# Performance work log

Measured on AMD Instinct MI355X. Metric: run time of the kernel, lower is better.

## Reference

```python
import jax, jax.numpy as jnp
import numpy as np

H = 128

def _lstm_dir(x, w_ih, w_hh, b_ih, b_hh, reverse):
    # x: [B,T,D]; w_ih: [4H,D]; w_hh: [4H,H]; gate order i,f,g,o (PyTorch)
    B = x.shape[0]
    pre = jnp.einsum('btd,gd->btg', x, w_ih) + b_ih + b_hh  # [B,T,4H]
    if reverse:
        pre = pre[:, ::-1]
    pre = jnp.swapaxes(pre, 0, 1)  # [T,B,4H]
    h0 = jnp.zeros((B, H), dtype=x.dtype)
    c0 = jnp.zeros((B, H), dtype=x.dtype)

    def step(carry, xt):
        h, c = carry
        gates = xt + h @ w_hh.T
        i, f, g, o = jnp.split(gates, 4, axis=-1)
        c = jax.nn.sigmoid(f) * c + jax.nn.sigmoid(i) * jnp.tanh(g)
        h = jax.nn.sigmoid(o) * jnp.tanh(c)
        return (h, c), h

    _, hs = jax.lax.scan(step, (h0, c0), pre)  # hs: [T,B,H]
    hs = jnp.swapaxes(hs, 0, 1)  # [B,T,H]
    if reverse:
        hs = hs[:, ::-1]
    return hs

def _bilstm_layer(x, wf, rf):
    fwd = _lstm_dir(x, *wf, reverse=False)
    bwd = _lstm_dir(x, *rf, reverse=True)
    return jnp.concatenate([fwd, bwd], axis=-1)

def setup_inputs() -> dict:
    key = jax.random.key(0)
    ks = jax.random.split(key, 32)
    s = 0.05
    d = {'x': jax.random.normal(ks[0], (64, 512, 64), dtype=jnp.float32)}
    i = 1
    for l, din in [(0, 64), (1, 2 * H)]:
        for suf in ['', 'r']:
            d[f'w_ih_l{l}{suf}'] = s * jax.random.normal(ks[i], (4 * H, din)); i += 1
            d[f'w_hh_l{l}{suf}'] = s * jax.random.normal(ks[i], (4 * H, H)); i += 1
            d[f'b_ih_l{l}{suf}'] = s * jax.random.normal(ks[i], (4 * H,)); i += 1
            d[f'b_hh_l{l}{suf}'] = s * jax.random.normal(ks[i], (4 * H,)); i += 1
    d['w_fc'] = s * jax.random.normal(ks[i], (64, 2 * H)); i += 1
    d['b_fc'] = s * jax.random.normal(ks[i], (64,))
    return d

def reference(x, w_ih_l0, w_hh_l0, b_ih_l0, b_hh_l0, w_ih_l0r, w_hh_l0r, b_ih_l0r, b_hh_l0r, w_ih_l1, w_hh_l1, b_ih_l1, b_hh_l1, w_ih_l1r, w_hh_l1r, b_ih_l1r, b_hh_l1r, w_fc, b_fc):
    h = _bilstm_layer(x, (w_ih_l0, w_hh_l0, b_ih_l0, b_hh_l0), (w_ih_l0r, w_hh_l0r, b_ih_l0r, b_hh_l0r))
    h = _bilstm_layer(h, (w_ih_l1, w_hh_l1, b_ih_l1, b_hh_l1), (w_ih_l1r, w_hh_l1r, b_ih_l1r, b_hh_l1r))
    return h @ w_fc.T + b_fc
```

## Files before the change

### kernel.cpp

```cpp
#include <hip/hip_runtime.h>

#define TT 512
#define BB 64
#define HH 128
#define G4 512
#define PF 4

typedef short bf16x8 __attribute__((ext_vector_type(8)));
typedef short s16x4  __attribute__((ext_vector_type(4)));
typedef float f32x4  __attribute__((ext_vector_type(4)));
typedef _Float16 f16x8v __attribute__((ext_vector_type(8)));

__device__ __forceinline__ unsigned short f2bf(float x) {
    unsigned u = __float_as_uint(x);
    u += 0x7fff + ((u >> 16) & 1);
    return (unsigned short)(u >> 16);
}
__device__ __forceinline__ float bf2f(unsigned short h) {
    return __uint_as_float(((unsigned)h) << 16);
}

__global__ __launch_bounds__(256) void convert_hilo(
    const float4* __restrict__ src, s16x4* __restrict__ hi,
    s16x4* __restrict__ lo, int n4)
{
    for (int i = blockIdx.x * 256 + threadIdx.x; i < n4; i += gridDim.x * 256) {
        float4 f = src[i];
        float fa[4] = {f.x, f.y, f.z, f.w};
        s16x4 h, l;
        #pragma unroll
        for (int e = 0; e < 4; ++e) {
            unsigned short hh = f2bf(fa[e]);
            h[e] = (short)hh;
            l[e] = (short)f2bf(fa[e] - bf2f(hh));
        }
        hi[i] = h;
        lo[i] = l;
    }
}

template<int K>
__global__ __launch_bounds__(256) void gemm_mfma2(
    const short* __restrict__ Ahi, const short* __restrict__ Alo,
    const float* __restrict__ W,
    const float* __restrict__ b0, const float* __restrict__ b1,
    float* __restrict__ C)
{
    constexpr int NC  = K / 32;
    constexpr int LDA = 40;
    __shared__ short Ahi_s[128 * LDA], Alo_s[128 * LDA];
    __shared__ short Whi_s[128 * LDA], Wlo_s[128 * LDA];

    const int bm  = blockIdx.x * 128;
    const int bn  = blockIdx.y * 128;
    const int tid = threadIdx.x;
    const int wv  = tid >> 6;
    const int l   = tid & 63;
    const int jl  = l & 15;
    const int rg  = l >> 4;
    const int wr  = wv >> 1;
    const int wc  = wv & 1;

    const int sr = tid >> 1;
    const int sc = (tid & 1) * 16;

    const short* Aph = Ahi + (size_t)(bm + sr) * K + sc;
    const short* Apl = Alo + (size_t)(bm + sr) * K + sc;
    const float* Wp  = W   + (size_t)(bn + sr) * K + sc;

    f32x4 acc[4][4];
    #pragma unroll
    for (int i = 0; i < 4; ++i)
        #pragma unroll
        for (int j = 0; j < 4; ++j)
            acc[i][j] = (f32x4){0.f, 0.f, 0.f, 0.f};

    bf16x8 pah[2], pal[2];
    float4 pw[4];
    pah[0] = *(const bf16x8*)(Aph);
    pah[1] = *(const bf16x8*)(Aph + 8);
    pal[0] = *(const bf16x8*)(Apl);
    pal[1] = *(const bf16x8*)(Apl + 8);
    #pragma unroll
    for (int q = 0; q < 4; ++q) pw[q] = *(const float4*)(Wp + q * 4);

    #pragma unroll 1
    for (int c = 0; c < NC; ++c) {
        __syncthreads();
        {
            int off = sr * LDA + sc;
            *(bf16x8*)&Ahi_s[off]     = pah[0];
            *(bf16x8*)&Ahi_s[off + 8] = pah[1];
            *(bf16x8*)&Alo_s[off]     = pal[0];
            *(bf16x8*)&Alo_s[off + 8] = pal[1];
            #pragma unroll
            for (int q = 0; q < 4; ++q) {
                float fw[4] = {pw[q].x, pw[q].y, pw[q].z, pw[q].w};
                s16x4 h, lo4;
                #pragma unroll
                for (int e = 0; e < 4; ++e) {
                    unsigned short hh = f2bf(fw[e]);
                    h[e]   = (short)hh;
                    lo4[e] = (short)f2bf(fw[e] - bf2f(hh));
                }
                *(s16x4*)&Whi_s[off + q * 4] = h;
                *(s16x4*)&Wlo_s[off + q * 4] = lo4;
            }
        }
        __syncthreads();
        if (c + 1 < NC) {
            pah[0] = *(const bf16x8*)(Aph + (c + 1) * 32);
            pah[1] = *(const bf16x8*)(Aph + (c + 1) * 32 + 8);
            pal[0] = *(const bf16x8*)(Apl + (c + 1) * 32);
            pal[1] = *(const bf16x8*)(Apl + (c + 1) * 32 + 8);
            #pragma unroll
            for (int q = 0; q < 4; ++q)
                pw[q] = *(const float4*)(Wp + (c + 1) * 32 + q * 4);
        }
        bf16x8 ah[4], al[4], wh[4], wl[4];
        #pragma unroll
        for (int t = 0; t < 4; ++t) {
            int ra = (wr * 64 + t * 16 + jl) * LDA + rg * 8;
            ah[t] = *(const bf16x8*)&Ahi_s[ra];
            al[t] = *(const bf16x8*)&Alo_s[ra];
            int rw = (wc * 64 + t * 16 + jl) * LDA + rg * 8;
            wh[t] = *(const bf16x8*)&Whi_s[rw];
            wl[t] = *(const bf16x8*)&Wlo_s[rw];
        }
        #pragma unroll
        for (int tm = 0; tm < 4; ++tm)
            #pragma unroll
            for (int tn = 0; tn < 4; ++tn) {
                acc[tm][tn] = __builtin_amdgcn_mfma_f32_16x16x32_bf16(ah[tm], wh[tn], acc[tm][tn], 0, 0, 0);
                acc[tm][tn] = __builtin_amdgcn_mfma_f32_16x16x32_bf16(ah[tm], wl[tn], acc[tm][tn], 0, 0, 0);
                acc[tm][tn] = __builtin_amdgcn_mfma_f32_16x16x32_bf16(al[tm], wh[tn], acc[tm][tn], 0, 0, 0);
            }
    }

    #pragma unroll
    for (int tn = 0; tn < 4; ++tn) {
        int n = bn + wc * 64 + tn * 16 + jl;
        float bias = b0[n] + b1[n];
        #pragma unroll
        for (int tm = 0; tm < 4; ++tm) {
            int m = bm + wr * 64 + tm * 16 + rg * 4;
            #pragma unroll
            for (int r = 0; r < 4; ++r)
                C[(size_t)(m + r) * G4 + n] = acc[tm][tn][r] + bias;
        }
    }
}

__global__ __launch_bounds__(512) void lstm_scan_v12(
    const float* __restrict__ pre_f, const float* __restrict__ pre_b,
    const float* __restrict__ whh_f, const float* __restrict__ whh_b,
    float* __restrict__ out)
{
    const int dir = blockIdx.x >> 6;
    const int b   = blockIdx.x & 63;
    const float* __restrict__ pre  = dir ? pre_b : pre_f;
    const float* __restrict__ w_hh = dir ? whh_b : whh_f;

    const int tid = threadIdx.x;
    const int w   = tid >> 6;
    const int l   = tid & 63;
    const int jl  = l & 15;
    const int rg  = l >> 4;

    __shared__ _Float16 h_lds[2][HH];
    __shared__ float oring[2][PF][HH];

    f16x8v bw[4][4];
    #pragma unroll
    for (int cc = 0; cc < 4; ++cc) {
        const float* wr_ = w_hh + (size_t)(cc * HH + w * 16 + jl) * HH + rg * 8;
        #pragma unroll
        for (int kc = 0; kc < 4; ++kc) {
            const float* p_ = wr_ + kc * 32;
            f16x8v f;
            #pragma unroll
            for (int e = 0; e < 8; ++e) f[e] = (_Float16)p_[e];
            bw[cc][kc] = f;
        }
    }

    if (tid < 2 * HH) ((_Float16*)h_lds)[tid] = (_Float16)0.f;

    const size_t base = (size_t)b * TT * G4 + w * 16 + jl;
    float pf[PF][4];
    #pragma unroll
    for (int u = 0; u < PF; ++u) {
        int tau = dir ? (TT - 1 - u) : u;
        #pragma unroll
        for (int cc = 0; cc < 4; ++cc)
            pf[u][cc] = pre[base + (size_t)tau * G4 + cc * HH];
    }

    float c = 0.f;
    const float ASIG = -1.4426950408889634f;
    const float ATAN =  2.8853900817779268f;

    const int s_loc = tid >> 7;
    const int c128  = tid & 127;

    __syncthreads();

    for (int s0 = 0; s0 < TT; s0 += PF) {
        const int p = (s0 >> 2) & 1;
        #pragma unroll
        for (int u = 0; u < PF; ++u) {
            const int s = s0 + u;
            const int cur = u & 1;

            f16x8v a[4];
            #pragma unroll
            for (int kc = 0; kc < 4; ++kc)
                a[kc] = *(const f16x8v*)&h_lds[cur][kc * 32 + rg * 8];

            f32x4 acc[4];
            #pragma unroll
            for (int cc = 0; cc < 4; ++cc)
                acc[cc] = (f32x4){pf[u][cc], 0.f, 0.f, 0.f};

            {
                int sn = s + PF;
                int taun = dir ? (TT - 1 - sn) : sn;
                taun = taun < 0 ? 0 : (taun > TT - 1 ? TT - 1 : taun);
                #pragma unroll
                for (int cc = 0; cc < 4; ++cc)
                    pf[u][cc] = pre[base + (size_t)taun * G4 + cc * HH];
            }

            #pragma unroll
            for (int cc = 0; cc < 4; ++cc)
                #pragma unroll
                for (int kc = 0; kc < 4; ++kc)
                    acc[cc] = __builtin_amdgcn_mfma_f32_16x16x32_f16(
                        a[kc], bw[cc][kc], acc[cc], 0, 0, 0);

            if (l < 16) {
                float gi = acc[0][0], gf = acc[1][0], gg = acc[2][0], go = acc[3][0];
                float ei = __builtin_amdgcn_exp2f(ASIG * gi);
                float si = __builtin_amdgcn_rcpf(1.f + ei);
                float ef = __builtin_amdgcn_exp2f(ASIG * gf);
                float sf = __builtin_amdgcn_rcpf(1.f + ef);
                float eg = __builtin_amdgcn_exp2f(ATAN * gg);
                float tg = 1.f - 2.f * __builtin_amdgcn_rcpf(1.f + eg);
                float eo = __builtin_amdgcn_exp2f(ASIG * go);
                float so = __builtin_amdgcn_rcpf(1.f + eo);
                c = fmaf(sf, c, si * tg);
                float e2 = __builtin_amdgcn_exp2f(ATAN * c);
                float h  = so * (1.f - 2.f * __builtin_amdgcn_rcpf(1.f + e2));
                int j = w * 16 + l;
                h_lds[cur ^ 1][j] = (_Float16)h;
                oring[p][u][j] = h;
            }
            __syncthreads();
        }

        {
            int sb = s0 + s_loc;
            int tau = dir ? (TT - 1 - sb) : sb;
            out[((size_t)b * TT + tau) * (2 * HH) + dir * HH + c128] =
                oring[p][s_loc][c128];
        }
    }
}

__global__ __launch_bounds__(256) void fc_v2(
    const float* __restrict__ h2, const float* __restrict__ w_fc,
    const float* __restrict__ b_fc, float* __restrict__ out)
{
    __shared__ float4 wsT[64][64];
    const int tid = threadIdx.x;
    const int bm  = blockIdx.x * 64;
    const int n   = tid & 63;
    const int mg  = tid >> 6;

    #pragma unroll
    for (int qq = 0; qq < 16; ++qq) {
        int id = qq * 256 + tid;
        int nn = id >> 6, k4 = id & 63;
        wsT[k4][nn] = *(const float4*)&w_fc[(size_t)nn * 256 + k4 * 4];
    }
    __syncthreads();

    const float bias = b_fc[n];
    const float* hrow = h2 + (size_t)(bm + mg * 16) * 256;

    float acc[16];
    #pragma unroll
    for (int mi = 0; mi < 16; ++mi) acc[mi] = 0.f;

    #pragma unroll 2
    for (int k4 = 0; k4 < 64; ++k4) {
        float4 w4 = wsT[k4][n];
        #pragma unroll
        for (int mi = 0; mi < 16; ++mi) {
            float4 h4 = *(const float4*)(hrow + (size_t)mi * 256 + k4 * 4);
            acc[mi] = fmaf(h4.x, w4.x, acc[mi]);
            acc[mi] = fmaf(h4.y, w4.y, acc[mi]);
            acc[mi] = fmaf(h4.z, w4.z, acc[mi]);
            acc[mi] = fmaf(h4.w, w4.w, acc[mi]);
        }
    }
    #pragma unroll
    for (int mi = 0; mi < 16; ++mi)
        out[(size_t)(bm + mg * 16 + mi) * 64 + n] = acc[mi] + bias;
}

extern "C" void kernel_launch(void* const* d_in, const int* in_sizes, int n_in,
                              void* d_out, int out_size, void* d_ws, size_t ws_size,
                              hipStream_t stream) {
    const float* x        = (const float*)d_in[0];
    const float* w_ih_l0  = (const float*)d_in[1];
    const float* w_hh_l0  = (const float*)d_in[2];
    const float* b_ih_l0  = (const float*)d_in[3];
    const float* b_hh_l0  = (const float*)d_in[4];
    const float* w_ih_l0r = (const float*)d_in[5];
    const float* w_hh_l0r = (const float*)d_in[6];
    const float* b_ih_l0r = (const float*)d_in[7];
    const float* b_hh_l0r = (const float*)d_in[8];
    const float* w_ih_l1  = (const float*)d_in[9];
    const float* w_hh_l1  = (const float*)d_in[10];
    const float* b_ih_l1  = (const float*)d_in[11];
    const float* b_hh_l1  = (const float*)d_in[12];
    const float* w_ih_l1r = (const float*)d_in[13];
    const float* w_hh_l1r = (const float*)d_in[14];
    const float* b_ih_l1r = (const float*)d_in[15];
    const float* b_hh_l1r = (const float*)d_in[16];
    const float* w_fc     = (const float*)d_in[17];
    const float* b_fc     = (const float*)d_in[18];

    float* ws    = (float*)d_ws;
    float* pre_f = ws;
    float* pre_b = ws + 16777216;
    float* out0  = ws + 2 * 16777216;
    float* out1  = out0 + 8388608;

    short* xhi  = (short*)out0;
    short* xlo  = xhi + 2097152;
    short* a1hi = (short*)out1;
    short* a1lo = a1hi + 8388608;

    dim3 gg(256, 4);

    convert_hilo<<<2048, 256, 0, stream>>>((const float4*)x, (s16x4*)xhi, (s16x4*)xlo, 524288);
    gemm_mfma2<64><<<gg, 256, 0, stream>>>(xhi, xlo, w_ih_l0,  b_ih_l0,  b_hh_l0,  pre_f);
    gemm_mfma2<64><<<gg, 256, 0, stream>>>(xhi, xlo, w_ih_l0r, b_ih_l0r, b_hh_l0r, pre_b);
    lstm_scan_v12<<<128, 512, 0, stream>>>(pre_f, pre_b, w_hh_l0, w_hh_l0r, out0);

    convert_hilo<<<2048, 256, 0, stream>>>((const float4*)out0, (s16x4*)a1hi, (s16x4*)a1lo, 2097152);
    gemm_mfma2<256><<<gg, 256, 0, stream>>>(a1hi, a1lo, w_ih_l1,  b_ih_l1,  b_hh_l1,  pre_f);
    gemm_mfma2<256><<<gg, 256, 0, stream>>>(a1hi, a1lo, w_ih_l1r, b_ih_l1r, b_hh_l1r, pre_b);
    lstm_scan_v12<<<128, 512, 0, stream>>>(pre_f, pre_b, w_hh_l1, w_hh_l1r, out1);

    fc_v2<<<512, 256, 0, stream>>>(out1, w_fc, b_fc, (float*)d_out);
}
```

Before: 682.5 us.

## Halve LSTM scan block to 4 waves, each computing two hidden tiles

The recurrent scan kernel now uses 256 threads (4 waves) per block instead of 512, and each wave owns 32 hidden units instead of 16. Each wave holds twice as many W_hh fragments in registers and issues twice the MFMAs per step. The aim is to make each per-step __syncthreads barrier cheaper across fewer waves. The cost is a longer serial MFMA chain and more gate math per wave, plus higher register pressure that the (256,1) launch bound is meant to allow.

```diff
diff --git a/kernel.cpp b/kernel.cpp
--- a/kernel.cpp
+++ b/kernel.cpp
@@ -151,7 +151,7 @@
     }
 }
 
-__global__ __launch_bounds__(512) void lstm_scan_v12(
+__global__ __launch_bounds__(256, 1) void lstm_scan_v13(
     const float* __restrict__ pre_f, const float* __restrict__ pre_b,
     const float* __restrict__ whh_f, const float* __restrict__ whh_b,
     float* __restrict__ out)
@@ -170,38 +170,42 @@
     __shared__ _Float16 h_lds[2][HH];
     __shared__ float oring[2][PF][HH];
 
-    f16x8v bw[4][4];
-    #pragma unroll
-    for (int cc = 0; cc < 4; ++cc) {
-        const float* wr_ = w_hh + (size_t)(cc * HH + w * 16 + jl) * HH + rg * 8;
-        #pragma unroll
-        for (int kc = 0; kc < 4; ++kc) {
-            const float* p_ = wr_ + kc * 32;
-            f16x8v f;
-            #pragma unroll
-            for (int e = 0; e < 8; ++e) f[e] = (_Float16)p_[e];
-            bw[cc][kc] = f;
-        }
-    }
+    f16x8v bw[4][2][4];
+    #pragma unroll
+    for (int cc = 0; cc < 4; ++cc)
+        #pragma unroll
+        for (int tt = 0; tt < 2; ++tt) {
+            const float* wr_ = w_hh + (size_t)(cc * HH + w * 32 + tt * 16 + jl) * HH + rg * 8;
+            #pragma unroll
+            for (int kc = 0; kc < 4; ++kc) {
+                const float* p_ = wr_ + kc * 32;
+                f16x8v f;
+                #pragma unroll
+                for (int e = 0; e < 8; ++e) f[e] = (_Float16)p_[e];
+                bw[cc][tt][kc] = f;
+            }
+        }
 
     if (tid < 2 * HH) ((_Float16*)h_lds)[tid] = (_Float16)0.f;
 
-    const size_t base = (size_t)b * TT * G4 + w * 16 + jl;
-    float pf[PF][4];
+    const size_t base = (size_t)b * TT * G4 + w * 32 + jl;
+    float pf[PF][4][2];
     #pragma unroll
     for (int u = 0; u < PF; ++u) {
         int tau = dir ? (TT - 1 - u) : u;
         #pragma unroll
         for (int cc = 0; cc < 4; ++cc)
-            pf[u][cc] = pre[base + (size_t)tau * G4 + cc * HH];
-    }
-
-    float c = 0.f;
+            #pragma unroll
+            for (int tt = 0; tt < 2; ++tt)
+                pf[u][cc][tt] = pre[base + (size_t)tau * G4 + cc * HH + tt * 16];
+    }
+
+    float cst[2] = {0.f, 0.f};
     const float ASIG = -1.4426950408889634f;
     const float ATAN =  2.8853900817779268f;
 
-    const int s_loc = tid >> 7;
-    const int c128  = tid & 127;
+    const int s_loc = tid >> 6;
+    const int c64   = tid & 63;
 
     __syncthreads();
 
@@ -217,10 +221,12 @@
             for (int kc = 0; kc < 4; ++kc)
                 a[kc] = *(const f16x8v*)&h_lds[cur][kc * 32 + rg * 8];
 
-            f32x4 acc[4];
+            f32x4 acc[4][2];
             #pragma unroll
             for (int cc = 0; cc < 4; ++cc)
-                acc[cc] = (f32x4){pf[u][cc], 0.f, 0.f, 0.f};
+                #pragma unroll
+                for (int tt = 0; tt < 2; ++tt)
+                    acc[cc][tt] = (f32x4){pf[u][cc][tt], 0.f, 0.f, 0.f};
 
             {
                 int sn = s + PF;
@@ -228,32 +234,41 @@
                 taun = taun < 0 ? 0 : (taun > TT - 1 ? TT - 1 : taun);
                 #pragma unroll
                 for (int cc = 0; cc < 4; ++cc)
-                    pf[u][cc] = pre[base + (size_t)taun * G4 + cc * HH];
+                    #pragma unroll
+                    for (int tt = 0; tt < 2; ++tt)
+                        pf[u][cc][tt] = pre[base + (size_t)taun * G4 + cc * HH + tt * 16];
             }
 
             #pragma unroll
             for (int cc = 0; cc < 4; ++cc)
                 #pragma unroll
-                for (int kc = 0; kc < 4; ++kc)
-                    acc[cc] = __builtin_amdgcn_mfma_f32_16x16x32_f16(
-                        a[kc], bw[cc][kc], acc[cc], 0, 0, 0);
+                for (int tt = 0; tt < 2; ++tt)
+                    #pragma unroll
+                    for (int kc = 0; kc < 4; ++kc)
+                        acc[cc][tt] = __builtin_amdgcn_mfma_f32_16x16x32_f16(
+                            a[kc], bw[cc][tt][kc], acc[cc][tt], 0, 0, 0);
 
             if (l < 16) {
-                float gi = acc[0][0], gf = acc[1][0], gg = acc[2][0], go = acc[3][0];
-                float ei = __builtin_amdgcn_exp2f(ASIG * gi);
-                float si = __builtin_amdgcn_rcpf(1.f + ei);
-                float ef = __builtin_amdgcn_exp2f(ASIG * gf);
-                float sf = __builtin_amdgcn_rcpf(1.f + ef);
-                float eg = __builtin_amdgcn_exp2f(ATAN * gg);
-                float tg = 1.f - 2.f * __builtin_amdgcn_rcpf(1.f + eg);
-                float eo = __builtin_amdgcn_exp2f(ASIG * go);
-                float so = __builtin_amdgcn_rcpf(1.f + eo);
-                c = fmaf(sf, c, si * tg);
-                float e2 = __builtin_amdgcn_exp2f(ATAN * c);
-                float h  = so * (1.f - 2.f * __builtin_amdgcn_rcpf(1.f + e2));
-                int j = w * 16 + l;
-                h_lds[cur ^ 1][j] = (_Float16)h;
-                oring[p][u][j] = h;
+                #pragma unroll
+                for (int tt = 0; tt < 2; ++tt) {
+                    float gi = acc[0][tt][0], gf = acc[1][tt][0];
+                    float gg = acc[2][tt][0], go = acc[3][tt][0];
+                    float ei = __builtin_amdgcn_exp2f(ASIG * gi);
+                    float si = __builtin_amdgcn_rcpf(1.f + ei);
+                    float ef = __builtin_amdgcn_exp2f(ASIG * gf);
+                    float sf = __builtin_amdgcn_rcpf(1.f + ef);
+                    float eg = __builtin_amdgcn_exp2f(ATAN * gg);
+                    float tg = 1.f - 2.f * __builtin_amdgcn_rcpf(1.f + eg);
+                    float eo = __builtin_amdgcn_exp2f(ASIG * go);
+                    float so = __builtin_amdgcn_rcpf(1.f + eo);
+                    float c  = fmaf(sf, cst[tt], si * tg);
+                    cst[tt] = c;
+                    float e2 = __builtin_amdgcn_exp2f(ATAN * c);
+                    float h  = so * (1.f - 2.f * __builtin_amdgcn_rcpf(1.f + e2));
+                    int j = w * 32 + tt * 16 + l;
+                    h_lds[cur ^ 1][j] = (_Float16)h;
+                    oring[p][u][j] = h;
+                }
             }
             __syncthreads();
         }
@@ -261,8 +276,9 @@
         {
             int sb = s0 + s_loc;
             int tau = dir ? (TT - 1 - sb) : sb;
-            out[((size_t)b * TT + tau) * (2 * HH) + dir * HH + c128] =
-                oring[p][s_loc][c128];
+            float* orow = out + ((size_t)b * TT + tau) * (2 * HH) + dir * HH;
+            orow[c64]      = oring[p][s_loc][c64];
+            orow[c64 + 64] = oring[p][s_loc][c64 + 64];
         }
     }
 }
@@ -348,12 +364,12 @@
     convert_hilo<<<2048, 256, 0, stream>>>((const float4*)x, (s16x4*)xhi, (s16x4*)xlo, 524288);
     gemm_mfma2<64><<<gg, 256, 0, stream>>>(xhi, xlo, w_ih_l0,  b_ih_l0,  b_hh_l0,  pre_f);
     gemm_mfma2<64><<<gg, 256, 0, stream>>>(xhi, xlo, w_ih_l0r, b_ih_l0r, b_hh_l0r, pre_b);
-    lstm_scan_v12<<<128, 512, 0, stream>>>(pre_f, pre_b, w_hh_l0, w_hh_l0r, out0);
+    lstm_scan_v13<<<128, 256, 0, stream>>>(pre_f, pre_b, w_hh_l0, w_hh_l0r, out0);
 
     convert_hilo<<<2048, 256, 0, stream>>>((const float4*)out0, (s16x4*)a1hi, (s16x4*)a1lo, 2097152);
     gemm_mfma2<256><<<gg, 256, 0, stream>>>(a1hi, a1lo, w_ih_l1,  b_ih_l1,  b_hh_l1,  pre_f);
     gemm_mfma2<256><<<gg, 256, 0, stream>>>(a1hi, a1lo, w_ih_l1r, b_ih_l1r, b_hh_l1r, pre_b);
-    lstm_scan_v12<<<128, 512, 0, stream>>>(pre_f, pre_b, w_hh_l1, w_hh_l1r, out1);
+    lstm_scan_v13<<<128, 256, 0, stream>>>(pre_f, pre_b, w_hh_l1, w_hh_l1r, out1);
 
     fc_v2<<<512, 256, 0, stream>>>(out1, w_fc, b_fc, (float*)d_out);
 }
```

Measured after the change: 807.2 us. 18.3% more time.

## Pre-split input weights to bf16 hi/lo once and relax LSTM step barrier

Applied to the files above, without the earlier changes.

Input-projection weights are now converted to bf16 hi/lo pairs in four small kernels up front, staged in the output buffer, so each GEMM block loads ready bf16 data instead of reconverting fp32 weights every tile. This cuts redundant conversion ALU work and halves weight load bytes in the GEMMs. Separately, the per-timestep __syncthreads in the LSTM scan is replaced by a barrier that waits only on LDS counters, not outstanding global memory ops, to shorten the serial recurrence. The relaxed barrier assumes no global writes need ordering across the step, and the staging relies on the FC kernel overwriting d_out last.

```diff
diff --git a/kernel.cpp b/kernel.cpp
--- a/kernel.cpp
+++ b/kernel.cpp
@@ -18,6 +18,10 @@
 }
 __device__ __forceinline__ float bf2f(unsigned short h) {
     return __uint_as_float(((unsigned)h) << 16);
+}
+
+__device__ __forceinline__ void barrier_lds_only() {
+    asm volatile("s_waitcnt lgkmcnt(0)\n\ts_barrier" ::: "memory");
 }
 
 __global__ __launch_bounds__(256) void convert_hilo(
@@ -40,9 +44,9 @@
 }
 
 template<int K>
-__global__ __launch_bounds__(256) void gemm_mfma2(
+__global__ __launch_bounds__(256) void gemm_mfma3(
     const short* __restrict__ Ahi, const short* __restrict__ Alo,
-    const float* __restrict__ W,
+    const short* __restrict__ Whi, const short* __restrict__ Wlo,
     const float* __restrict__ b0, const float* __restrict__ b1,
     float* __restrict__ C)
 {
@@ -66,7 +70,8 @@
 
     const short* Aph = Ahi + (size_t)(bm + sr) * K + sc;
     const short* Apl = Alo + (size_t)(bm + sr) * K + sc;
-    const float* Wp  = W   + (size_t)(bn + sr) * K + sc;
+    const short* Wph = Whi + (size_t)(bn + sr) * K + sc;
+    const short* Wpl = Wlo + (size_t)(bn + sr) * K + sc;
 
     f32x4 acc[4][4];
     #pragma unroll
@@ -75,14 +80,11 @@
         for (int j = 0; j < 4; ++j)
             acc[i][j] = (f32x4){0.f, 0.f, 0.f, 0.f};
 
-    bf16x8 pah[2], pal[2];
-    float4 pw[4];
-    pah[0] = *(const bf16x8*)(Aph);
-    pah[1] = *(const bf16x8*)(Aph + 8);
-    pal[0] = *(const bf16x8*)(Apl);
-    pal[1] = *(const bf16x8*)(Apl + 8);
-    #pragma unroll
-    for (int q = 0; q < 4; ++q) pw[q] = *(const float4*)(Wp + q * 4);
+    bf16x8 pah[2], pal[2], pwh[2], pwl[2];
+    pah[0] = *(const bf16x8*)(Aph);     pah[1] = *(const bf16x8*)(Aph + 8);
+    pal[0] = *(const bf16x8*)(Apl);     pal[1] = *(const bf16x8*)(Apl + 8);
+    pwh[0] = *(const bf16x8*)(Wph);     pwh[1] = *(const bf16x8*)(Wph + 8);
+    pwl[0] = *(const bf16x8*)(Wpl);     pwl[1] = *(const bf16x8*)(Wpl + 8);
 
     #pragma unroll 1
     for (int c = 0; c < NC; ++c) {
@@ -93,19 +95,10 @@
             *(bf16x8*)&Ahi_s[off + 8] = pah[1];
             *(bf16x8*)&Alo_s[off]     = pal[0];
             *(bf16x8*)&Alo_s[off + 8] = pal[1];
-            #pragma unroll
-            for (int q = 0; q < 4; ++q) {
-                float fw[4] = {pw[q].x, pw[q].y, pw[q].z, pw[q].w};
-                s16x4 h, lo4;
-                #pragma unroll
-                for (int e = 0; e < 4; ++e) {
-                    unsigned short hh = f2bf(fw[e]);
-                    h[e]   = (short)hh;
-                    lo4[e] = (short)f2bf(fw[e] - bf2f(hh));
-                }
-                *(s16x4*)&Whi_s[off + q * 4] = h;
-                *(s16x4*)&Wlo_s[off + q * 4] = lo4;
-            }
+            *(bf16x8*)&Whi_s[off]     = pwh[0];
+            *(bf16x8*)&Whi_s[off + 8] = pwh[1];
+            *(bf16x8*)&Wlo_s[off]     = pwl[0];
+            *(bf16x8*)&Wlo_s[off + 8] = pwl[1];
         }
         __syncthreads();
         if (c + 1 < NC) {
@@ -113,9 +106,10 @@
             pah[1] = *(const bf16x8*)(Aph + (c + 1) * 32 + 8);
             pal[0] = *(const bf16x8*)(Apl + (c + 1) * 32);
             pal[1] = *(const bf16x8*)(Apl + (c + 1) * 32 + 8);
-            #pragma unroll
-            for (int q = 0; q < 4; ++q)
-                pw[q] = *(const float4*)(Wp + (c + 1) * 32 + q * 4);
+            pwh[0] = *(const bf16x8*)(Wph + (c + 1) * 32);
+            pwh[1] = *(const bf16x8*)(Wph + (c + 1) * 32 + 8);
+            pwl[0] = *(const bf16x8*)(Wpl + (c + 1) * 32);
+            pwl[1] = *(const bf16x8*)(Wpl + (c + 1) * 32 + 8);
         }
         bf16x8 ah[4], al[4], wh[4], wl[4];
         #pragma unroll
@@ -151,7 +145,7 @@
     }
 }
 
-__global__ __launch_bounds__(512) void lstm_scan_v12(
+__global__ __launch_bounds__(512) void lstm_scan_v14(
     const float* __restrict__ pre_f, const float* __restrict__ pre_b,
     const float* __restrict__ whh_f, const float* __restrict__ whh_b,
     float* __restrict__ out)
@@ -255,7 +249,7 @@
                 h_lds[cur ^ 1][j] = (_Float16)h;
                 oring[p][u][j] = h;
             }
-            __syncthreads();
+            barrier_lds_only();
         }
 
         {
@@ -343,17 +337,28 @@
     short* a1hi = (short*)out1;
     short* a1lo = a1hi + 8388608;
 
+    short* wsp    = (short*)d_out;
+    short* w0f_hi = wsp;              short* w0f_lo = wsp + 32768;
+    short* w0r_hi = wsp + 65536;      short* w0r_lo = wsp + 98304;
+    short* w1f_hi = wsp + 131072;     short* w1f_lo = wsp + 262144;
+    short* w1r_hi = wsp + 393216;     short* w1r_lo = wsp + 524288;
+
     dim3 gg(256, 4);
 
+    convert_hilo<<<32,  256, 0, stream>>>((const float4*)w_ih_l0,  (s16x4*)w0f_hi, (s16x4*)w0f_lo, 8192);
+    convert_hilo<<<32,  256, 0, stream>>>((const float4*)w_ih_l0r, (s16x4*)w0r_hi, (s16x4*)w0r_lo, 8192);
+    convert_hilo<<<128, 256, 0, stream>>>((const float4*)w_ih_l1,  (s16x4*)w1f_hi, (s16x4*)w1f_lo, 32768);
+    convert_hilo<<<128, 256, 0, stream>>>((const float4*)w_ih_l1r, (s16x4*)w1r_hi, (s16x4*)w1r_lo, 32768);
+
     convert_hilo<<<2048, 256, 0, stream>>>((const float4*)x, (s16x4*)xhi, (s16x4*)xlo, 524288);
-    gemm_mfma2<64><<<gg, 256, 0, stream>>>(xhi, xlo, w_ih_l0,  b_ih_l0,  b_hh_l0,  pre_f);
-    gemm_mfma2<64><<<gg, 256, 0, stream>>>(xhi, xlo, w_ih_l0r, b_ih_l0r, b_hh_l0r, pre_b);
-    lstm_scan_v12<<<128, 512, 0, stream>>>(pre_f, pre_b, w_hh_l0, w_hh_l0r, out0);
+    gemm_mfma3<64><<<gg, 256, 0, stream>>>(xhi, xlo, w0f_hi, w0f_lo, b_ih_l0,  b_hh_l0,  pre_f);
+    gemm_mfma3<64><<<gg, 256, 0, stream>>>(xhi, xlo, w0r_hi, w0r_lo, b_ih_l0r, b_hh_l0r, pre_b);
+    lstm_scan_v14<<<128, 512, 0, stream>>>(pre_f, pre_b, w_hh_l0, w_hh_l0r, out0);
 
     convert_hilo<<<2048, 256, 0, stream>>>((const float4*)out0, (s16x4*)a1hi, (s16x4*)a1lo, 2097152);
-    gemm_mfma2<256><<<gg, 256, 0, stream>>>(a1hi, a1lo, w_ih_l1,  b_ih_l1,  b_hh_l1,  pre_f);
-    gemm_mfma2<256><<<gg, 256, 0, stream>>>(a1hi, a1lo, w_ih_l1r, b_ih_l1r, b_hh_l1r, pre_b);
-    lstm_scan_v12<<<128, 512, 0, stream>>>(pre_f, pre_b, w_hh_l1, w_hh_l1r, out1);
+    gemm_mfma3<256><<<gg, 256, 0, stream>>>(a1hi, a1lo, w1f_hi, w1f_lo, b_ih_l1,  b_hh_l1,  pre_f);
+    gemm_mfma3<256><<<gg, 256, 0, stream>>>(a1hi, a1lo, w1r_hi, w1r_lo, b_ih_l1r, b_hh_l1r, pre_b);
+    lstm_scan_v14<<<128, 512, 0, stream>>>(pre_f, pre_b, w_hh_l1, w_hh_l1r, out1);
 
     fc_v2<<<512, 256, 0, stream>>>(out1, w_fc, b_fc, (float*)d_out);
 }
```

Result: no change. 694.7 us (+1.8%).
